# Optimization experiments

Hardware: AMD Instinct MI355X
Metric: run time of the kernel (lower is better)

Reference implementation:

```python
import jax, jax.numpy as jnp
import numpy as np
from jax import lax

# ---- config (mirrors cfg.* used by the module) ----
ANCHOR_RATIOS = (0.5, 1.0, 2.0)
ANCHOR_SCALES = (8.0, 16.0, 32.0)
FEATURE_STRIDE = 16
BASE_SIZE = 40  # generate_anchors(40, ...)
BN_EPS = 1e-5
LOG_CLAMP = 1e-30  # torch uses 1e-300, which underflows to 0 in fp32; use fp32-safe tiny


def generate_anchors(base_size=BASE_SIZE, ratios=ANCHOR_RATIOS, scales=ANCHOR_SCALES):
    """py-faster-rcnn style anchor generation, corner format (x1,y1,x2,y2). -> (A,4)"""
    w = h = float(base_size)
    cx = (base_size - 1) * 0.5
    cy = (base_size - 1) * 0.5
    size = w * h
    out = []
    for r in ratios:
        ws = np.round(np.sqrt(size / r))
        hs = np.round(ws * r)
        for s in scales:
            W, H = ws * s, hs * s
            out.append([cx - 0.5 * (W - 1), cy - 0.5 * (H - 1),
                        cx + 0.5 * (W - 1), cy + 0.5 * (H - 1)])
    return np.asarray(out, dtype=np.float32)  # (A,4)


def splash_anchors(fH, fW, n, base_anchors, stride):
    """Shift base anchors over the feature grid. -> (n, fH*fW*A, 4), row-major H,W then A."""
    sx = jnp.arange(fW, dtype=jnp.float32) * stride
    sy = jnp.arange(fH, dtype=jnp.float32) * stride
    SY, SX = jnp.meshgrid(sy, sx, indexing='ij')            # (fH,fW)
    shifts = jnp.stack([SX, SY, SX, SY], axis=-1).reshape(-1, 1, 4)  # (fH*fW,1,4)
    anc = (shifts + jnp.asarray(base_anchors)[None, :, :]).reshape(-1, 4)  # (fH*fW*A,4)
    return jnp.broadcast_to(anc[None], (n, anc.shape[0], 4))


def conv2d(x, w, b, pad):
    y = lax.conv_general_dilated(x, w, (1, 1), [(pad, pad), (pad, pad)],
                                 dimension_numbers=('NCHW', 'OIHW', 'NCHW'))
    return y + b[None, :, None, None]


def batchnorm_train(x, gamma, beta):
    # training-mode BN: per-channel batch stats over (N,H,W), biased variance
    m = jnp.mean(x, axis=(0, 2, 3), keepdims=True)
    v = jnp.mean(jnp.square(x - m), axis=(0, 2, 3), keepdims=True)
    xn = (x - m) * lax.rsqrt(v + BN_EPS)
    return xn * gamma[None, :, None, None] + beta[None, :, None, None]


def mish(x):
    return x * jnp.tanh(jax.nn.softplus(x))


def corner2center(b):
    w = b[..., 2] - b[..., 0]
    h = b[..., 3] - b[..., 1]
    cx = b[..., 0] + 0.5 * w
    cy = b[..., 1] + 0.5 * h
    return jnp.stack([cx, cy, w, h], axis=-1)


def setup_inputs() -> dict:
    key = jax.random.key(0)
    ks = jax.random.split(key, 7)
    C_IN, C_BASE, A = 256, 256, 9
    x = jax.random.normal(ks[0], (8, C_IN, 128, 128), dtype=jnp.float32)
    # kaiming-uniform-ish scaled weights
    def kaiming(k, shape):
        fan_in = shape[1] * shape[2] * shape[3]
        bound = float(np.sqrt(6.0 / fan_in))
        return jax.random.uniform(k, shape, jnp.float32, -bound, bound)
    return {
        "x": x,
        "W_base": kaiming(ks[1], (C_BASE, C_IN, 3, 3)),
        "b_base": jnp.zeros((C_BASE,), jnp.float32),
        "g_base": jnp.ones((C_BASE,), jnp.float32),
        "be_base": jnp.zeros((C_BASE,), jnp.float32),
        "W_cls": kaiming(ks[2], (2 * A, C_BASE, 1, 1)),
        "b_cls": jnp.zeros((2 * A,), jnp.float32),
        "g_cls": jnp.ones((2 * A,), jnp.float32),
        "be_cls": jnp.zeros((2 * A,), jnp.float32),
        "W_reg": kaiming(ks[3], (4 * A, C_BASE, 1, 1)),
        "b_reg": jnp.zeros((4 * A,), jnp.float32),
        "g_reg": jnp.ones((4 * A,), jnp.float32),
        "be_reg": jnp.zeros((4 * A,), jnp.float32),
        "img_size": 2048,
    }


def reference(x, W_base, b_base, g_base, be_base,
              W_cls, b_cls, g_cls, be_cls,
              W_reg, b_reg, g_reg, be_reg, img_size):
    n, c, fH, fW = x.shape
    A = 9
    # BASE_CONV: Conv3x3 -> Mish -> Dropout2d (identity here, deterministic) -> BN
    base = batchnorm_train(mish(conv2d(x, W_base, b_base, 1)), g_base, be_base)

    anchors = splash_anchors(fH, fW, n, generate_anchors(), FEATURE_STRIDE)  # (n,K,4) corners

    rpn_reg = batchnorm_train(conv2d(base, W_reg, b_reg, 0), g_reg, be_reg)
    rpn_reg = jnp.transpose(rpn_reg, (0, 2, 3, 1)).reshape(n, -1, 4)          # (n,K,4)

    rpn_score = batchnorm_train(conv2d(base, W_cls, b_cls, 0), g_cls, be_cls)
    rpn_score = jnp.transpose(rpn_score, (0, 2, 3, 1)).reshape(n, fH, fW, A, 2)
    fg_scores = jax.nn.softmax(rpn_score, axis=4)[..., 1].reshape(n, -1)      # (n,K)

    rpn_reg = rpn_reg + anchors                                               # decoded corners

    # proposal layer: clip proposals to the image, keep all (fixed-shape)
    lim = jnp.float32(img_size)
    rois = jnp.clip(rpn_reg, 0.0, lim)                                        # (n,K,4) corners
    rois = corner2center(rois)                                                # (cx,cy,w,h)

    anc_c = corner2center(anchors)
    tx = (rois[..., 0] - anc_c[..., 0]) / anc_c[..., 2]
    ty = (rois[..., 1] - anc_c[..., 1]) / anc_c[..., 3]
    tw = jnp.log(jnp.maximum(rois[..., 2] / anc_c[..., 2], LOG_CLAMP))
    th = jnp.log(jnp.maximum(rois[..., 3] / anc_c[..., 3], LOG_CLAMP))
    ts = jnp.stack([tx, ty, tw, th], axis=-1)
    return (fg_scores, ts, rois)
```

## Files before the change

### kernel.cpp

```cpp
#include <hip/hip_runtime.h>
#include <stdint.h>

typedef short bf16x8 __attribute__((ext_vector_type(8)));
typedef float f32x4 __attribute__((ext_vector_type(4)));

#define AS1 __attribute__((address_space(1)))
#define AS3 __attribute__((address_space(3)))

static __device__ __forceinline__ void gl16(const void* g, void* l) {
  __builtin_amdgcn_global_load_lds((const AS1 void*)g, (AS3 void*)l, 16, 0, 0);
}

static __device__ __forceinline__ unsigned short f2bf(float f) {
  unsigned u = __float_as_uint(f);
  u = u + 0x7fffu + ((u >> 16) & 1u);
  return (unsigned short)(u >> 16);
}
static __device__ __forceinline__ float bf2f(unsigned short h) {
  return __uint_as_float(((unsigned)h) << 16);
}
static __device__ __forceinline__ float mishf(float x) {
  float sp = fmaxf(x, 0.f) + log1pf(expf(-fabsf(x)));
  float e2 = expf(-2.f * sp);
  float th = (1.f - e2) / (1.f + e2);
  return x * th;
}

#define NIMG 8
#define HH 128
#define WW 128
#define HP 130
#define CIN 256
#define MPIX (NIMG * HH * WW)
#define KTOT 2304
#define FGCNT (MPIX * 9)
#define TSCNT (MPIX * 9 * 4)

__device__ __constant__ float AW[9] = {456.f, 912.f, 1824.f, 320.f, 640.f, 1280.f, 224.f, 448.f, 896.f};
__device__ __constant__ float AH[9] = {224.f, 448.f, 896.f, 320.f, 640.f, 1280.f, 448.f, 896.f, 1792.f};

__global__ __launch_bounds__(256) void k_wt(const float* __restrict__ Wb,
                                            unsigned short* __restrict__ Wt2) {
  int d = blockIdx.x * 256 + threadIdx.x;
  int c = d & 31, oc = (d >> 5) & 255, s = d >> 13;
  int icb = s / 9, khw = s % 9, kh = khw / 3, kw = khw % 3;
  int ic = icb * 32 + c;
  Wt2[d] = f2bf(Wb[((oc * 256 + ic) * 3 + kh) * 3 + kw]);
}

__global__ __launch_bounds__(256) void k_tr(const float* __restrict__ x,
                                            unsigned short* __restrict__ xt2) {
  __shared__ float tile[32][129];
  int b = blockIdx.x;
  int icb = b & 7, h = (b >> 3) & 127, n = b >> 10;
  int t = threadIdx.x;
  const float* src = x + (((size_t)(n * 256 + icb * 32) * 128 + h) * 128);
#pragma unroll
  for (int i = 0; i < 4; ++i) {
    int idx = t + 256 * i;
    int w4 = idx & 31, ic = idx >> 5;
    float4 v = *(const float4*)(src + (size_t)ic * 16384 + w4 * 4);
    tile[ic][w4 * 4 + 0] = v.x; tile[ic][w4 * 4 + 1] = v.y;
    tile[ic][w4 * 4 + 2] = v.z; tile[ic][w4 * 4 + 3] = v.w;
  }
  __syncthreads();
#pragma unroll
  for (int i = 0; i < 8; ++i) {
    int idx = t + 256 * i;
    int icp = idx & 15, w = idx >> 4;
    unsigned lo = f2bf(tile[icp * 2][w]);
    unsigned hi = f2bf(tile[icp * 2 + 1][w]);
    size_t pix = ((size_t)(icb * 8 + n) * HP + (h + 1)) * HP + (w + 1);
    *(unsigned*)(xt2 + pix * 32 + icp * 2) = lo | (hi << 16);
  }
}

__global__ __launch_bounds__(256) void k_bord(unsigned short* __restrict__ xt2) {
  int tid = blockIdx.x * 256 + threadIdx.x;
  int chunk = tid & 3, pix = tid >> 2;
  int nn = pix / 516, bp = pix % 516;
  int hp, wp;
  if (bp < 130) { hp = 0; wp = bp; }
  else if (bp < 260) { hp = 129; wp = bp - 130; }
  else { int r = bp - 260; hp = 1 + (r >> 1); wp = (r & 1) ? 129 : 0; }
  size_t off = (((size_t)nn * HP + hp) * HP + wp) * 32 + chunk * 8;
  uint4 z = {0u, 0u, 0u, 0u};
  *(uint4*)(xt2 + off) = z;
}

__global__ __launch_bounds__(256) void k_conv(const unsigned short* __restrict__ xt2,
                                              const unsigned short* __restrict__ Wt2,
                                              const float* __restrict__ b_base,
                                              unsigned short* __restrict__ yt2,
                                              float* __restrict__ statsA) {
  __shared__ __align__(16) char lds[32768];
  int t = threadIdx.x;
  int lane = t & 63, w4 = t >> 6;
  int wr = w4 >> 1, wc = w4 & 1;
  int row16 = lane & 15, kgl = lane >> 4;
  int pr = lane & 15, pq = lane >> 4;

  int bid = blockIdx.x;
  int swz = (bid & 7) * 256 + (bid >> 3);
  int pixb = swz >> 1, oh = swz & 1;
  int n = pixb >> 7, h0 = pixb & 127;
  size_t M0 = (size_t)pixb * 128;

  f32x4 acc[4][4];
#pragma unroll
  for (int m = 0; m < 4; ++m)
#pragma unroll
    for (int nf = 0; nf < 4; ++nf) { f32x4 z = {0.f, 0.f, 0.f, 0.f}; acc[m][nf] = z; }

  const unsigned short* aS0 =
      xt2 + ((size_t)(n * HP + h0) * HP + w4 * 32 + pr) * 32 + pq * 8;
  const unsigned short* aS1 = aS0 + 16 * 32;
  const unsigned short* bS0 = Wt2 + (size_t)(oh * 128 + w4 * 32 + pr) * 32 + pq * 8;
  const unsigned short* bS1 = bS0 + 16 * 32;

  const size_t planeStride = (size_t)8 * HP * HP * 32;
  int aoffA = wr * 4096 + kgl * 256 + row16 * 16;
  int aoffB = wc * 4096 + kgl * 256 + row16 * 16;

  auto aoff32 = [&](int sl) -> size_t {
    int icb_ = (sl * 57) >> 9;
    int khw = sl - icb_ * 9;
    int kh_ = (khw * 11) >> 5;
    int kw_ = khw - kh_ * 3;
    return (size_t)icb_ * planeStride + ((size_t)kh_ * HP + kw_) * 32;
  };

  for (int s = 0; s < 36; ++s) {
#pragma unroll
    for (int kc = 0; kc < 2; ++kc) {
      int sl = 2 * s + kc;
      size_t offA = aoff32(sl);
      size_t offB = (size_t)sl * 8192;
      char* bufA = lds + kc * 8192;
      char* bufB = lds + 16384 + kc * 8192;
      gl16(aS0 + offA, bufA + (2 * w4) * 1024);
      gl16(aS1 + offA, bufA + (2 * w4 + 1) * 1024);
      gl16(bS0 + offB, bufB + (2 * w4) * 1024);
      gl16(bS1 + offB, bufB + (2 * w4 + 1) * 1024);
    }
    __syncthreads();
    bf16x8 af[4][2], bfr[4][2];
#pragma unroll
    for (int kc = 0; kc < 2; ++kc) {
#pragma unroll
      for (int m = 0; m < 4; ++m)
        af[m][kc] = *(const bf16x8*)(lds + kc * 8192 + aoffA + m * 1024);
#pragma unroll
      for (int nf = 0; nf < 4; ++nf)
        bfr[nf][kc] = *(const bf16x8*)(lds + 16384 + kc * 8192 + aoffB + nf * 1024);
    }
#pragma unroll
    for (int m = 0; m < 4; ++m)
#pragma unroll
      for (int nf = 0; nf < 4; ++nf) {
        acc[m][nf] = __builtin_amdgcn_mfma_f32_16x16x32_bf16(af[m][0], bfr[nf][0], acc[m][nf], 0, 0, 0);
        acc[m][nf] = __builtin_amdgcn_mfma_f32_16x16x32_bf16(af[m][1], bfr[nf][1], acc[m][nf], 0, 0, 0);
      }
    __syncthreads();
  }

  float sums[4] = {0.f, 0.f, 0.f, 0.f}, sumq[4] = {0.f, 0.f, 0.f, 0.f};
#pragma unroll
  for (int nf = 0; nf < 4; ++nf) {
    int oc = oh * 128 + wc * 64 + nf * 16 + row16;
    float bias = b_base[oc];
    size_t obase = (size_t)(oc >> 5) * MPIX * 32 + (oc & 31);
#pragma unroll
    for (int m = 0; m < 4; ++m) {
#pragma unroll
      for (int j = 0; j < 4; ++j) {
        int p = wr * 64 + m * 16 + kgl * 4 + j;
        float y = mishf(acc[m][nf][j] + bias);
        yt2[obase + (M0 + p) * 32] = f2bf(y);
        sums[nf] += y; sumq[nf] += y * y;
      }
    }
  }
#pragma unroll
  for (int nf = 0; nf < 4; ++nf) {
    float s1 = sums[nf], s2 = sumq[nf];
    s1 += __shfl_xor(s1, 16); s2 += __shfl_xor(s2, 16);
    s1 += __shfl_xor(s1, 32); s2 += __shfl_xor(s2, 32);
    if (lane < 16) {
      int oc = oh * 128 + wc * 64 + nf * 16 + lane;
      atomicAdd(&statsA[oc], s1);
      atomicAdd(&statsA[256 + oc], s2);
    }
  }
}

__global__ __launch_bounds__(256) void k_fold(const float* __restrict__ statsA,
                                              const float* __restrict__ g_base,
                                              const float* __restrict__ be_base,
                                              const float* __restrict__ W_cls,
                                              const float* __restrict__ b_cls,
                                              const float* __restrict__ W_reg,
                                              const float* __restrict__ b_reg,
                                              unsigned short* __restrict__ W2t2,
                                              float* __restrict__ b2) {
  __shared__ float sS[256], sT[256];
  int t = threadIdx.x;
  {
    float cnt = (float)MPIX;
    float m = statsA[t] / cnt;
    float v = fmaxf(statsA[256 + t] / cnt - m * m, 0.f);
    float s = g_base[t] * rsqrtf(v + 1e-5f);
    sS[t] = s;
    sT[t] = be_base[t] - m * s;
  }
  __syncthreads();
  if (t < 64) {
    float bias = 0.f;
    if (t < 36) bias = b_reg[t];
    else if (t < 54) bias = b_cls[t - 36];
    float acc = 0.f;
    for (int ic = 0; ic < 256; ++ic) {
      float w = 0.f;
      if (t < 36) w = W_reg[t * 256 + ic];
      else if (t < 54) w = W_cls[(t - 36) * 256 + ic];
      acc += w * sT[ic];
      W2t2[((size_t)(ic >> 5) * 64 + t) * 32 + (ic & 31)] = f2bf(w * sS[ic]);
    }
    b2[t] = bias + acc;
  }
}

__global__ __launch_bounds__(256) void k_mm2(const unsigned short* __restrict__ yt2,
                                             const unsigned short* __restrict__ W2t2,
                                             const float* __restrict__ b2,
                                             unsigned short* __restrict__ zt,
                                             float* __restrict__ statsZ) {
  __shared__ __align__(16) char lds2[24576];
  int t = threadIdx.x, lane = t & 63, w4 = t >> 6;
  int row16 = lane & 15, kgl = lane >> 4;
  int pr = lane & 15, pq = lane >> 4;
  size_t pixbase = (size_t)blockIdx.x * 128;

  f32x4 acc[2][4];
#pragma unroll
  for (int m = 0; m < 2; ++m)
#pragma unroll
    for (int nn = 0; nn < 4; ++nn) { f32x4 z = {0.f, 0.f, 0.f, 0.f}; acc[m][nn] = z; }

  const unsigned short* aS0 = yt2 + (pixbase + w4 * 32 + pr) * 32 + pq * 8;
  const unsigned short* aS1 = aS0 + 16 * 32;
  const unsigned short* bS = W2t2 + (size_t)(w4 * 16 + pr) * 32 + pq * 8;

  int aoffA = w4 * 2048 + kgl * 256 + row16 * 16;
  int aoffB = kgl * 256 + row16 * 16;

  auto STG = [&](int s, int c_) {
    size_t ao = (size_t)s * MPIX * 32;
    size_t bo = (size_t)s * 2048;
    char* buf = lds2 + c_ * 12288;
    gl16(aS0 + ao, buf + (2 * w4) * 1024);
    gl16(aS1 + ao, buf + (2 * w4 + 1) * 1024);
    gl16(bS + bo, buf + 8192 + w4 * 1024);
  };

  STG(0, 0);
  int cur = 0;
  for (int s = 0; s < 8; ++s) {
    __syncthreads();
    if (s < 7) STG(s + 1, cur ^ 1);
    const char* ab = lds2 + cur * 12288;
    const char* bb = ab + 8192;
    bf16x8 af[2], bfr[4];
#pragma unroll
    for (int m = 0; m < 2; ++m) af[m] = *(const bf16x8*)(ab + aoffA + m * 1024);
#pragma unroll
    for (int nn = 0; nn < 4; ++nn) bfr[nn] = *(const bf16x8*)(bb + aoffB + nn * 1024);
#pragma unroll
    for (int m = 0; m < 2; ++m)
#pragma unroll
      for (int nn = 0; nn < 4; ++nn)
        acc[m][nn] = __builtin_amdgcn_mfma_f32_16x16x32_bf16(af[m], bfr[nn], acc[m][nn], 0, 0, 0);
    cur ^= 1;
  }

  float sums[4] = {0.f, 0.f, 0.f, 0.f}, sumq[4] = {0.f, 0.f, 0.f, 0.f};
#pragma unroll
  for (int nn = 0; nn < 4; ++nn) {
    int oc = nn * 16 + row16;
    float bias = b2[oc];
#pragma unroll
    for (int m = 0; m < 2; ++m) {
#pragma unroll
      for (int j = 0; j < 4; ++j) {
        int p = w4 * 32 + m * 16 + kgl * 4 + j;
        float v = acc[m][nn][j] + bias;
        zt[(pixbase + p) * 64 + oc] = f2bf(v);
        sums[nn] += v; sumq[nn] += v * v;
      }
    }
  }
#pragma unroll
  for (int nn = 0; nn < 4; ++nn) {
    float s1 = sums[nn], s2 = sumq[nn];
    s1 += __shfl_xor(s1, 16); s2 += __shfl_xor(s2, 16);
    s1 += __shfl_xor(s1, 32); s2 += __shfl_xor(s2, 32);
    if (lane < 16) {
      int oc = nn * 16 + lane;
      atomicAdd(&statsZ[oc], s1);
      atomicAdd(&statsZ[64 + oc], s2);
    }
  }
}

__global__ __launch_bounds__(64) void k_zstat(const float* __restrict__ statsZ,
                                              const float* __restrict__ g_cls,
                                              const float* __restrict__ be_cls,
                                              const float* __restrict__ g_reg,
                                              const float* __restrict__ be_reg,
                                              float* __restrict__ zsc,
                                              float* __restrict__ zsh) {
  int t = threadIdx.x;
  float g = 1.f, be = 0.f;
  if (t < 36) { g = g_reg[t]; be = be_reg[t]; }
  else if (t < 54) { g = g_cls[t - 36]; be = be_cls[t - 36]; }
  float cnt = (float)MPIX;
  float m = statsZ[t] / cnt;
  float v = fmaxf(statsZ[64 + t] / cnt - m * m, 0.f);
  float s = g * rsqrtf(v + 1e-5f);
  zsc[t] = s;
  zsh[t] = be - m * s;
}

__global__ __launch_bounds__(256) void k_dec(const unsigned short* __restrict__ zt,
                                             const float* __restrict__ zsc,
                                             const float* __restrict__ zsh,
                                             const int* __restrict__ imgsz,
                                             float* __restrict__ out) {
  int p = blockIdx.x * 256 + threadIdx.x;
  float lim = (float)imgsz[0];
  float zn[64];
  {
    const uint4* zp4 = (const uint4*)(zt + (size_t)p * 64);
#pragma unroll
    for (int i = 0; i < 8; ++i) {
      uint4 v = zp4[i];
      unsigned a0 = v.x, a1 = v.y, a2 = v.z, a3 = v.w;
      zn[i * 8 + 0] = bf2f((unsigned short)(a0 & 0xffff));
      zn[i * 8 + 1] = bf2f((unsigned short)(a0 >> 16));
      zn[i * 8 + 2] = bf2f((unsigned short)(a1 & 0xffff));
      zn[i * 8 + 3] = bf2f((unsigned short)(a1 >> 16));
      zn[i * 8 + 4] = bf2f((unsigned short)(a2 & 0xffff));
      zn[i * 8 + 5] = bf2f((unsigned short)(a2 >> 16));
      zn[i * 8 + 6] = bf2f((unsigned short)(a3 & 0xffff));
      zn[i * 8 + 7] = bf2f((unsigned short)(a3 >> 16));
    }
#pragma unroll
    for (int i = 0; i < 54; ++i) zn[i] = zn[i] * zsc[i] + zsh[i];
  }
  int rem = p & 16383, h = rem >> 7, w = rem & 127;
  float fx = 16.f * (float)w, fy = 16.f * (float)h;
  size_t kbase = (size_t)p * 9;
  float* fgout = out;
  float* tsout = out + FGCNT;
  float* roout = out + FGCNT + TSCNT;
#pragma unroll
  for (int a = 0; a < 9; ++a) {
    float x1 = 20.f - 0.5f * AW[a] + fx;
    float y1 = 20.f - 0.5f * AH[a] + fy;
    float x2 = 19.f + 0.5f * AW[a] + fx;
    float y2 = 19.f + 0.5f * AH[a] + fy;
    float cx1 = fminf(fmaxf(x1 + zn[4 * a + 0], 0.f), lim);
    float cy1 = fminf(fmaxf(y1 + zn[4 * a + 1], 0.f), lim);
    float cx2 = fminf(fmaxf(x2 + zn[4 * a + 2], 0.f), lim);
    float cy2 = fminf(fmaxf(y2 + zn[4 * a + 3], 0.f), lim);
    float bw = cx2 - cx1, bh = cy2 - cy1;
    float cx = cx1 + 0.5f * bw, cy = cy1 + 0.5f * bh;
    float aw = AW[a] - 1.f, ah = AH[a] - 1.f;
    float acx = 19.5f + fx, acy = 19.5f + fy;
    float tx = (cx - acx) / aw, ty = (cy - acy) / ah;
    float tw = logf(fmaxf(bw / aw, 1e-30f));
    float th = logf(fmaxf(bh / ah, 1e-30f));
    float s0 = zn[36 + 2 * a], s1 = zn[36 + 2 * a + 1];
    float fg = 1.f / (1.f + expf(s0 - s1));
    fgout[kbase + a] = fg;
    size_t o4 = (kbase + a) * 4;
    tsout[o4 + 0] = tx; tsout[o4 + 1] = ty; tsout[o4 + 2] = tw; tsout[o4 + 3] = th;
    roout[o4 + 0] = cx; roout[o4 + 1] = cy; roout[o4 + 2] = bw; roout[o4 + 3] = bh;
  }
}

extern "C" void kernel_launch(void* const* d_in, const int* in_sizes, int n_in,
                              void* d_out, int out_size, void* d_ws, size_t ws_size,
                              hipStream_t stream) {
  const float* x   = (const float*)d_in[0];
  const float* Wb  = (const float*)d_in[1];
  const float* bb  = (const float*)d_in[2];
  const float* gb  = (const float*)d_in[3];
  const float* beb = (const float*)d_in[4];
  const float* Wc  = (const float*)d_in[5];
  const float* bc  = (const float*)d_in[6];
  const float* gc  = (const float*)d_in[7];
  const float* bec = (const float*)d_in[8];
  const float* Wr  = (const float*)d_in[9];
  const float* br  = (const float*)d_in[10];
  const float* gr  = (const float*)d_in[11];
  const float* ber = (const float*)d_in[12];
  const int* imgsz = (const int*)d_in[13];

  char* ws = (char*)d_ws;
  const size_t OFF_XTP = 0;
  const size_t OFF_Y   = 69222400;
  const size_t OFF_Z   = 136331264;
  const size_t OFF_WT  = 153108480;
  const size_t OFF_W2  = 154288128;
  const size_t OFF_S   = 154320896;
  unsigned short* xt2  = (unsigned short*)(ws + OFF_XTP);
  unsigned short* yt2  = (unsigned short*)(ws + OFF_Y);
  unsigned short* zt   = (unsigned short*)(ws + OFF_Z);
  unsigned short* Wt2  = (unsigned short*)(ws + OFF_WT);
  unsigned short* W2t2 = (unsigned short*)(ws + OFF_W2);
  float* b2     = (float*)(ws + OFF_S);
  float* statsA = (float*)(ws + OFF_S + 256);
  float* statsZ = (float*)(ws + OFF_S + 2304);
  float* zsc    = (float*)(ws + OFF_S + 2816);
  float* zsh    = (float*)(ws + OFF_S + 3072);
  float* out = (float*)d_out;

  hipMemsetAsync(statsA, 0, (512 + 128) * sizeof(float), stream);
  k_wt  <<<2304, 256, 0, stream>>>(Wb, Wt2);
  k_tr  <<<8192, 256, 0, stream>>>(x, xt2);
  k_bord<<<516, 256, 0, stream>>>(xt2);
  k_conv<<<2048, 256, 0, stream>>>(xt2, Wt2, bb, yt2, statsA);
  k_fold<<<1, 256, 0, stream>>>(statsA, gb, beb, Wc, bc, Wr, br, W2t2, b2);
  k_mm2 <<<1024, 256, 0, stream>>>(yt2, W2t2, b2, zt, statsZ);
  k_zstat<<<1, 64, 0, stream>>>(statsZ, gc, bec, gr, ber, zsc, zsh);
  k_dec <<<512, 256, 0, stream>>>(zt, zsc, zsh, imgsz, out);
}
```

Measured before the change: 594.6 us.

## Reuse one loaded input row across the three kw taps in the conv loop

Measured after the change: 554.4 us. 6.8% less time.

```diff
diff --git a/kernel.cpp b/kernel.cpp
--- a/kernel.cpp
+++ b/kernel.cpp
@@ -93,7 +93,9 @@
                                               const float* __restrict__ b_base,
                                               unsigned short* __restrict__ yt2,
                                               float* __restrict__ statsA) {
-  __shared__ __align__(16) char lds[32768];
+  __shared__ __align__(16) char lds[33792];
+  char* ldsA = lds;
+  char* ldsB = lds + 9216;
   int t = threadIdx.x;
   int lane = t & 63, w4 = t >> 6;
   int wr = w4 >> 1, wc = w4 & 1;
@@ -112,56 +114,44 @@
 #pragma unroll
     for (int nf = 0; nf < 4; ++nf) { f32x4 z = {0.f, 0.f, 0.f, 0.f}; acc[m][nf] = z; }
 
-  const unsigned short* aS0 =
-      xt2 + ((size_t)(n * HP + h0) * HP + w4 * 32 + pr) * 32 + pq * 8;
-  const unsigned short* aS1 = aS0 + 16 * 32;
-  const unsigned short* bS0 = Wt2 + (size_t)(oh * 128 + w4 * 32 + pr) * 32 + pq * 8;
-  const unsigned short* bS1 = bS0 + 16 * 32;
-
-  const size_t planeStride = (size_t)8 * HP * HP * 32;
-  int aoffA = wr * 4096 + kgl * 256 + row16 * 16;
-  int aoffB = wc * 4096 + kgl * 256 + row16 * 16;
-
-  auto aoff32 = [&](int sl) -> size_t {
-    int icb_ = (sl * 57) >> 9;
-    int khw = sl - icb_ * 9;
-    int kh_ = (khw * 11) >> 5;
-    int kw_ = khw - kh_ * 3;
-    return (size_t)icb_ * planeStride + ((size_t)kh_ * HP + kw_) * 32;
-  };
-
-  for (int s = 0; s < 36; ++s) {
-#pragma unroll
-    for (int kc = 0; kc < 2; ++kc) {
-      int sl = 2 * s + kc;
-      size_t offA = aoff32(sl);
-      size_t offB = (size_t)sl * 8192;
-      char* bufA = lds + kc * 8192;
-      char* bufB = lds + 16384 + kc * 8192;
-      gl16(aS0 + offA, bufA + (2 * w4) * 1024);
-      gl16(aS1 + offA, bufA + (2 * w4 + 1) * 1024);
-      gl16(bS0 + offB, bufB + (2 * w4) * 1024);
-      gl16(bS1 + offB, bufB + (2 * w4 + 1) * 1024);
-    }
-    __syncthreads();
-    bf16x8 af[4][2], bfr[4][2];
-#pragma unroll
-    for (int kc = 0; kc < 2; ++kc) {
-#pragma unroll
-      for (int m = 0; m < 4; ++m)
-        af[m][kc] = *(const bf16x8*)(lds + kc * 8192 + aoffA + m * 1024);
-#pragma unroll
-      for (int nf = 0; nf < 4; ++nf)
-        bfr[nf][kc] = *(const bf16x8*)(lds + 16384 + kc * 8192 + aoffB + nf * 1024);
-    }
-#pragma unroll
-    for (int m = 0; m < 4; ++m)
-#pragma unroll
-      for (int nf = 0; nf < 4; ++nf) {
-        acc[m][nf] = __builtin_amdgcn_mfma_f32_16x16x32_bf16(af[m][0], bfr[nf][0], acc[m][nf], 0, 0, 0);
-        acc[m][nf] = __builtin_amdgcn_mfma_f32_16x16x32_bf16(af[m][1], bfr[nf][1], acc[m][nf], 0, 0, 0);
+  const size_t planeStride = (size_t)HP * HP * 32;
+  int laneOffA = pr * 32 + pq * 8;
+
+  for (int icb = 0; icb < 8; ++icb) {
+    for (int kh = 0; kh < 3; ++kh) {
+      const unsigned short* aRow =
+          xt2 + (size_t)((icb * 8 + n) * HP + h0 + kh) * HP * 32;
+      gl16(aRow + w4 * 512 + laneOffA, ldsA + w4 * 1024);
+      gl16(aRow + (w4 + 4) * 512 + laneOffA, ldsA + (w4 + 4) * 1024);
+      if (w4 == 0) gl16(aRow + 8 * 512 + laneOffA, ldsA + 8 * 1024);
+      int slb = icb * 9 + kh * 3;
+#pragma unroll
+      for (int j = 0; j < 6; ++j) {
+        int g = w4 + 4 * j;
+        int kw_ = g >> 3, gg = g & 7;
+        gl16(Wt2 + ((size_t)(slb + kw_) * 256 + oh * 128 + gg * 16 + pr) * 32 + pq * 8,
+             ldsB + g * 1024);
       }
-    __syncthreads();
+      __syncthreads();
+#pragma unroll
+      for (int kw = 0; kw < 3; ++kw) {
+        bf16x8 af[4], bfr[4];
+#pragma unroll
+        for (int m = 0; m < 4; ++m) {
+          int p = wr * 64 + m * 16 + row16 + kw;
+          af[m] = *(const bf16x8*)(ldsA + (p >> 4) * 1024 + kgl * 256 + (p & 15) * 16);
+        }
+#pragma unroll
+        for (int nf = 0; nf < 4; ++nf)
+          bfr[nf] = *(const bf16x8*)(ldsB + (kw * 8 + wc * 4 + nf) * 1024 + kgl * 256 + row16 * 16);
+#pragma unroll
+        for (int m = 0; m < 4; ++m)
+#pragma unroll
+          for (int nf = 0; nf < 4; ++nf)
+            acc[m][nf] = __builtin_amdgcn_mfma_f32_16x16x32_bf16(af[m], bfr[nf], acc[m][nf], 0, 0, 0);
+      }
+      __syncthreads();
+    }
   }
 
   float sums[4] = {0.f, 0.f, 0.f, 0.f}, sumq[4] = {0.f, 0.f, 0.f, 0.f};
```
